# Optimization experiments

Measured on AMD Instinct MI355X. Metric: run time of the kernel, lower is better.

The kernel has to match this reference:

```python
import jax, jax.numpy as jnp
import numpy as np

B, T, D, SPAN = 4, 4096, 1024, 128


def _windowed_attention(q, k, v, span):
    # Causal sliding-window attention: position t attends to [max(0, t-span+1), t].
    # Tiled as blocks of size span: each query block attends to its own block
    # plus the previous block (exactly covers the window), avoiding any [T,T]
    # or per-timestep materialization.
    B, T, D = q.shape
    S = span
    nb = T // S  # T chosen divisible by span
    qb = q.reshape(B, nb, S, D)
    kb = k.reshape(B, nb, S, D)
    vb = v.reshape(B, nb, S, D)
    pad = jnp.zeros((B, 1, S, D), dtype=q.dtype)
    kk = jnp.concatenate([jnp.concatenate([pad, kb[:, :-1]], axis=1), kb], axis=2)  # [B,nb,2S,D]
    vv = jnp.concatenate([jnp.concatenate([pad, vb[:, :-1]], axis=1), vb], axis=2)  # [B,nb,2S,D]
    scale = 1.0 / jnp.sqrt(jnp.asarray(D, dtype=q.dtype))
    scores = jnp.einsum('bnqd,bnkd->bnqk', qb, kk) * scale  # [B,nb,S,2S]
    n_idx = jnp.arange(nb)[:, None, None]      # block index
    q_idx = jnp.arange(S)[None, :, None]       # query offset within block
    k_idx = jnp.arange(2 * S)[None, None, :]   # key offset in [prev|cur] pair
    rel = k_idx - S - q_idx                    # key_pos - query_pos
    # window: -span+1 <= rel <= 0; first block's "previous" half is padding -> mask it
    mask = (rel <= 0) & (rel > -S) & ((n_idx > 0) | (k_idx >= S))
    neg = jnp.asarray(jnp.finfo(scores.dtype).min, dtype=scores.dtype)
    scores = jnp.where(mask, scores, neg)
    w = jax.nn.softmax(scores, axis=-1)
    out = jnp.einsum('bnqk,bnkd->bnqd', w, vv)
    return out.reshape(B, T, D)


def setup_inputs() -> dict:
    key = jax.random.key(0)
    ks = jax.random.split(key, 7)
    s = 1.0 / np.sqrt(D)
    return {
        'x': jax.random.normal(ks[0], (B, T, D), dtype=jnp.float32),
        'Wq': jax.random.normal(ks[1], (D, D), dtype=jnp.float32) * s,
        'bq': jax.random.normal(ks[2], (D,), dtype=jnp.float32) * s,
        'Wk': jax.random.normal(ks[3], (D, D), dtype=jnp.float32) * s,
        'bk': jax.random.normal(ks[4], (D,), dtype=jnp.float32) * s,
        'Wv': jax.random.normal(ks[5], (D, D), dtype=jnp.float32) * s,
        'bv': jax.random.normal(ks[6], (D,), dtype=jnp.float32) * s,
        'span': SPAN,
    }


def reference(x, Wq, bq, Wk, bk, Wv, bv, span):
    # torch nn.Linear: y = x @ W.T + b
    q = jnp.einsum('btd,ed->bte', x, Wq) + bq
    k = jnp.einsum('btd,ed->bte', x, Wk) + bk
    v = jnp.einsum('btd,ed->bte', x, Wv) + bv
    return _windowed_attention(q, k, v, span)
```

## Files before the change

### kernel.cpp

```cpp
#include <hip/hip_runtime.h>
#include <hip/hip_bf16.h>

#define BB 4
#define TT 4096
#define DD 1024
#define SS 128
#define NBLK 32
#define MM (BB*TT)

typedef __attribute__((ext_vector_type(8))) short bf16x8;
typedef __attribute__((ext_vector_type(4))) short s16x4;
typedef __attribute__((ext_vector_type(4))) float f32x4;

#define VMCNT(N) asm volatile("s_waitcnt vmcnt(" #N ")" ::: "memory")

__device__ __forceinline__ void block_sync() {
    asm volatile("" ::: "memory");
    __builtin_amdgcn_s_barrier();
    asm volatile("" ::: "memory");
}

__device__ __forceinline__ short f2bf(float f) {
    union { float f; unsigned u; } cv; cv.f = f;
    unsigned u = cv.u;
    u += 0x7fffu + ((u >> 16) & 1u);
    return (short)(u >> 16);
}

__device__ __forceinline__ void gload16(const short* g, short* l) {
    __builtin_amdgcn_global_load_lds(
        (const __attribute__((address_space(1))) void*)g,
        (__attribute__((address_space(3))) void*)l, 16, 0, 0);
}

__global__ __launch_bounds__(256) void cast_f32_bf16(
    const float* __restrict__ src, short* __restrict__ dst)
{
    const int i = (blockIdx.x * 256 + threadIdx.x) * 4;
    const float4 v = *(const float4*)(src + i);
    s16x4 o;
    o.x = f2bf(v.x); o.y = f2bf(v.y); o.z = f2bf(v.z); o.w = f2bf(v.w);
    *(s16x4*)(dst + i) = o;
}

__global__ __launch_bounds__(256) void cast_w3(
    const float* __restrict__ a, const float* __restrict__ b,
    const float* __restrict__ c, short* __restrict__ dst)
{
    const float* src = (blockIdx.y == 0) ? a : (blockIdx.y == 1) ? b : c;
    short* d = dst + (size_t)blockIdx.y * DD * DD;
    const int i = (blockIdx.x * 256 + threadIdx.x) * 4;
    const float4 v = *(const float4*)(src + i);
    s16x4 o;
    o.x = f2bf(v.x); o.y = f2bf(v.y); o.z = f2bf(v.z); o.w = f2bf(v.w);
    *(s16x4*)(d + i) = o;
}

__global__ __launch_bounds__(256) void qkv_gemm(
    const short* __restrict__ X,
    const short* __restrict__ W3,
    const float* __restrict__ bq, const float* __restrict__ bk,
    const float* __restrict__ bv,
    short* __restrict__ q, short* __restrict__ k, short* __restrict__ vT)
{
    __shared__ short As[2][4096];
    __shared__ short Bs[2][4096];

    const int tid = threadIdx.x;
    const int l   = blockIdx.x;
    const int xcd = l & 7;
    const int rr  = l >> 3;
    const int m0  = (xcd * 16 + (rr & 15)) * 128;
    const int n_idx = rr >> 4;
    const int grp = n_idx >> 3;
    const int n0g = (n_idx & 7) * 128;

    const short* W = W3 + (size_t)grp * DD * DD;
    const float* bias = (grp == 0) ? bq : (grp == 1) ? bk : bv;

    const int wv   = tid >> 6, lane = tid & 63;
    const int wm   = wv >> 1,  wn   = wv & 1;
    const int quad = lane >> 4, c16 = lane & 15;
    const int srow = lane >> 2;
    const int scol = (lane & 3) * 8;

    auto stage = [&](int kk) {
        short* as = As[kk & 1];
        short* bs = Bs[kk & 1];
        const int k0 = kk * 32;
#pragma unroll
        for (int s = 0; s < 2; s++) {
            const int row = (wv * 2 + s) * 16 + srow;
            gload16(X + (m0 + row) * DD + k0 + scol, as + row * 32 + scol);
            gload16(W + (n0g + row) * DD + k0 + scol, bs + row * 32 + scol);
        }
    };

    f32x4 acc[4][4];
#pragma unroll
    for (int i = 0; i < 4; i++)
#pragma unroll
        for (int j = 0; j < 4; j++) acc[i][j] = (f32x4){0.f, 0.f, 0.f, 0.f};

    stage(0);

    if (grp != 2) {
        for (int kk = 0; kk < 32; kk++) {
            __syncthreads();
            if (kk < 31) stage(kk + 1);
            const short* as = As[kk & 1];
            const short* bs = Bs[kk & 1];
            bf16x8 af[4], bfr[4];
#pragma unroll
            for (int i = 0; i < 4; i++)
                af[i] = *(const bf16x8*)(as + (wm * 64 + i * 16 + c16) * 32 + quad * 8);
#pragma unroll
            for (int j = 0; j < 4; j++)
                bfr[j] = *(const bf16x8*)(bs + (wn * 64 + j * 16 + c16) * 32 + quad * 8);
#pragma unroll
            for (int i = 0; i < 4; i++)
#pragma unroll
                for (int j = 0; j < 4; j++)
                    acc[i][j] = __builtin_amdgcn_mfma_f32_16x16x32_bf16(af[i], bfr[j], acc[i][j], 0, 0, 0);
        }
        short* Y = (grp == 0) ? q : k;
#pragma unroll
        for (int j = 0; j < 4; j++) {
            const int col = n0g + wn * 64 + j * 16 + c16;
            const float bc = bias[col];
#pragma unroll
            for (int i = 0; i < 4; i++) {
                const int row = m0 + wm * 64 + i * 16 + quad * 4;
#pragma unroll
                for (int r = 0; r < 4; r++)
                    Y[(row + r) * DD + col] = f2bf(acc[i][j][r] + bc);
            }
        }
    } else {
        for (int kk = 0; kk < 32; kk++) {
            __syncthreads();
            if (kk < 31) stage(kk + 1);
            const short* as = As[kk & 1];
            const short* bs = Bs[kk & 1];
            bf16x8 af[4], bfr[4];
#pragma unroll
            for (int i = 0; i < 4; i++)
                af[i] = *(const bf16x8*)(as + (wm * 64 + i * 16 + c16) * 32 + quad * 8);
#pragma unroll
            for (int j = 0; j < 4; j++)
                bfr[j] = *(const bf16x8*)(bs + (wn * 64 + j * 16 + c16) * 32 + quad * 8);
#pragma unroll
            for (int i = 0; i < 4; i++)
#pragma unroll
                for (int j = 0; j < 4; j++)
                    acc[i][j] = __builtin_amdgcn_mfma_f32_16x16x32_bf16(bfr[j], af[i], acc[i][j], 0, 0, 0);
        }
        const int b  = m0 >> 12;
        const int t0 = m0 & 4095;
#pragma unroll
        for (int j = 0; j < 4; j++) {
#pragma unroll
            for (int r = 0; r < 4; r++) {
                const int drow = n0g + wn * 64 + j * 16 + quad * 4 + r;
                const float bc = bias[drow];
#pragma unroll
                for (int i = 0; i < 4; i++) {
                    const int tcol = t0 + wm * 64 + i * 16 + c16;
                    vT[(b * DD + drow) * TT + tcol] = f2bf(acc[i][j][r] + bc);
                }
            }
        }
    }
}

__global__ __launch_bounds__(256) void attn_fused(
    const short* __restrict__ Q,
    const short* __restrict__ Kb,
    const short* __restrict__ VT,
    float* __restrict__ O)
{
    __shared__ short lds[78336];

    const int l   = blockIdx.x;
    const int xcd = l & 7;
    const int rr  = l >> 3;
    const int n   = xcd * 4 + (rr & 3);
    const int qh  = (rr >> 2) & 1;
    const int b   = rr >> 3;

    const int tid  = threadIdx.x;
    const int wv   = tid >> 6, lane = tid & 63;
    const int quad = lane >> 4, c16 = lane & 15;
    const int srow = tid >> 2;
    const int scol = (tid & 3) * 8;

    const int qrow   = b * TT + n * SS + qh * 64;
    const int krow   = b * TT + n * SS - SS;
    const int bstart = b * TT;

    f32x4 acc[16];
#pragma unroll
    for (int j = 0; j < 16; j++) acc[j] = (f32x4){0.f, 0.f, 0.f, 0.f};

    auto stage1 = [&](int kk, int bi) {
        short* qb   = lds + bi * 20480;
        short* kbuf = qb + 4096;
        const int k0 = kk * 64;
#pragma unroll
        for (int ks = 0; ks < 2; ks++) {
            gload16(Q + (qrow + srow) * DD + k0 + ks * 32 + scol,
                    qb + ks * 2048 + srow * 32 + scol);
#pragma unroll
            for (int s = 0; s < 4; s++) {
                const int row = srow + s * 64;
                int g = krow + row;
                if (g < bstart) g = bstart;
                gload16(Kb + g * DD + k0 + ks * 32 + scol,
                        kbuf + ks * 8192 + row * 32 + scol);
            }
        }
    };

    stage1(0, 0);
    stage1(1, 1);
    for (int kk = 0; kk < 16; kk++) {
        if (kk < 15) { VMCNT(10); } else { VMCNT(0); }
        block_sync();
        if (kk < 14) stage1(kk + 2, (kk + 2) % 3);
        const short* qb   = lds + (kk % 3) * 20480;
        const short* kbuf = qb + 4096;
#pragma unroll
        for (int ks = 0; ks < 2; ks++) {
            bf16x8 a = *(const bf16x8*)(qb + ks * 2048 + (wv * 16 + c16) * 32 + quad * 8);
#pragma unroll
            for (int j = 0; j < 16; j++) {
                bf16x8 bf = *(const bf16x8*)(kbuf + ks * 8192 + (j * 16 + c16) * 32 + quad * 8);
                acc[j] = __builtin_amdgcn_mfma_f32_16x16x32_bf16(a, bf, acc[j], 0, 0, 0);
            }
        }
    }

    __syncthreads();

    const int tbase = n * SS - SS;
    auto stage2 = [&](int s, short* vbuf) {
        const int d0 = (s >> 1) * 128;
        const int kh = (s & 1) * 128;
#pragma unroll
        for (int kc = 0; kc < 4; kc++) {
#pragma unroll
            for (int s64 = 0; s64 < 2; s64++) {
                const int row = srow + s64 * 64;
                int t = tbase + kh + kc * 32 + scol;
                if (t < 0) t = 0;
                gload16(VT + (size_t)(b * DD + d0 + row) * TT + t,
                        vbuf + kc * 4096 + row * 32 + scol);
            }
        }
    };
    stage2(0, lds);
    stage2(1, lds + 16384);

    short* Pw = lds + 61440 + wv * (16 * 264);
    const float scale = 0.03125f;
#pragma unroll
    for (int r = 0; r < 4; r++) {
        const int q_idx = qh * 64 + wv * 16 + quad * 4 + r;
        float mx = -3.0e38f;
#pragma unroll
        for (int j = 0; j < 16; j++) {
            const int k_idx = j * 16 + c16;
            const int rel = k_idx - SS - q_idx;
            const bool valid = (rel <= 0) & (rel > -SS) & ((n > 0) | (k_idx >= SS));
            const float sv = valid ? acc[j][r] * scale : -3.0e38f;
            acc[j][r] = sv;
            mx = fmaxf(mx, sv);
        }
#pragma unroll
        for (int o = 1; o < 16; o <<= 1) mx = fmaxf(mx, __shfl_xor(mx, o));
        float sm = 0.f;
#pragma unroll
        for (int j = 0; j < 16; j++) {
            const float p = __expf(acc[j][r] - mx);
            acc[j][r] = p;
            sm += p;
        }
#pragma unroll
        for (int o = 1; o < 16; o <<= 1) sm += __shfl_xor(sm, o);
        const float inv = 1.0f / sm;
#pragma unroll
        for (int j = 0; j < 16; j++)
            Pw[(quad * 4 + r) * 264 + j * 16 + c16] = f2bf(acc[j][r] * inv);
    }

    f32x4 o8[8];
#pragma unroll
    for (int j = 0; j < 8; j++) o8[j] = (f32x4){0.f, 0.f, 0.f, 0.f};

    for (int s = 0; s < 16; s++) {
        if (s < 2)       { VMCNT(8); }
        else if (s < 15) { VMCNT(40); }
        else             { VMCNT(0); }
        block_sync();
        if (s < 14) stage2(s + 2, lds + ((s + 2) % 3) * 16384);
        const short* vbuf = lds + (s % 3) * 16384;
        const int kh = (s & 1) * 128;
#pragma unroll
        for (int kc = 0; kc < 4; kc++) {
            bf16x8 a = *(const bf16x8*)(Pw + c16 * 264 + kh + kc * 32 + quad * 8);
#pragma unroll
            for (int jj = 0; jj < 8; jj++) {
                bf16x8 bf = *(const bf16x8*)(vbuf + kc * 4096 + (jj * 16 + c16) * 32 + quad * 8);
                o8[jj] = __builtin_amdgcn_mfma_f32_16x16x32_bf16(a, bf, o8[jj], 0, 0, 0);
            }
        }
        if (s & 1) {
            const int d0 = (s >> 1) * 128;
#pragma unroll
            for (int jj = 0; jj < 8; jj++) {
#pragma unroll
                for (int r = 0; r < 4; r++)
                    O[(size_t)(qrow + wv * 16 + quad * 4 + r) * DD + d0 + jj * 16 + c16] = o8[jj][r];
                o8[jj] = (f32x4){0.f, 0.f, 0.f, 0.f};
            }
        }
    }
}

extern "C" void kernel_launch(void* const* d_in, const int* in_sizes, int n_in,
                              void* d_out, int out_size, void* d_ws, size_t ws_size,
                              hipStream_t stream) {
    const float* x  = (const float*)d_in[0];
    const float* Wq = (const float*)d_in[1];
    const float* bq = (const float*)d_in[2];
    const float* Wk = (const float*)d_in[3];
    const float* bk = (const float*)d_in[4];
    const float* Wv = (const float*)d_in[5];
    const float* bv = (const float*)d_in[6];
    float* out = (float*)d_out;

    char* ws = (char*)d_ws;
    const size_t SZ = (size_t)MM * DD * 2;
    short* q   = (short*)(ws);
    short* k   = (short*)(ws + SZ);
    short* vT  = (short*)(ws + 2 * SZ);
    short* xb  = (short*)(ws + 3 * SZ);
    short* w3b = (short*)(ws + 4 * SZ);

    dim3 blk(256);
    cast_f32_bf16<<<MM * DD / 1024, blk, 0, stream>>>(x, xb);
    cast_w3<<<dim3(DD * DD / 1024, 3), blk, 0, stream>>>(Wq, Wk, Wv, w3b);

    qkv_gemm<<<3072, blk, 0, stream>>>(xb, w3b, bq, bk, bv, q, k, vT);

    attn_fused<<<256, blk, 0, stream>>>(q, k, vT, out);
}
```

Before: 320.9 us.

## Rewrite QKV GEMM with 256x256 tiles, 8 waves, swizzled LDS and phased pipeline

Replaces the 128x128, 4-wave QKV projection GEMM with a templated 256x256-tile kernel using 512 threads, a 64-wide K step, XOR-swizzled LDS layout, and a four-phase schedule that interleaves async global-to-LDS staging with MFMA blocks under raised wave priority. Larger tiles raise arithmetic intensity and cut global traffic per FLOP, and the swizzle targets LDS bank conflicts. It also relaxes the final vmcnt wait in the attention kernel's last V stage from 0 to 16. The new GEMM uses many more accumulator registers and 128KB of LDS per block, and the relaxed wait could be unsafe if the outstanding loads are actually needed.

```diff
diff --git a/kernel.cpp b/kernel.cpp
--- a/kernel.cpp
+++ b/kernel.cpp
@@ -5,7 +5,6 @@
 #define TT 4096
 #define DD 1024
 #define SS 128
-#define NBLK 32
 #define MM (BB*TT)
 
 typedef __attribute__((ext_vector_type(8))) short bf16x8;
@@ -13,6 +12,7 @@
 typedef __attribute__((ext_vector_type(4))) float f32x4;
 
 #define VMCNT(N) asm volatile("s_waitcnt vmcnt(" #N ")" ::: "memory")
+#define LGKM0()  asm volatile("s_waitcnt lgkmcnt(0)" ::: "memory")
 
 __device__ __forceinline__ void block_sync() {
     asm volatile("" ::: "memory");
@@ -56,121 +56,168 @@
     *(s16x4*)(d + i) = o;
 }
 
-__global__ __launch_bounds__(256) void qkv_gemm(
-    const short* __restrict__ X,
-    const short* __restrict__ W3,
+
+#define MF(a_, b_, c_) ((GRP == 2)                                            \
+    ? __builtin_amdgcn_mfma_f32_16x16x32_bf16((b_), (a_), (c_), 0, 0, 0)      \
+    : __builtin_amdgcn_mfma_f32_16x16x32_bf16((a_), (b_), (c_), 0, 0, 0))
+
+#define QKV_PHASE(ABASE, P, STAGE_STMT, VM_STMT)                              \
+  do {                                                                        \
+    bf16x8 af0k0 = *(const bf16x8*)((ABASE) + (((P)*2)*16   + c16) * 64 + sw0);\
+    bf16x8 af0k1 = *(const bf16x8*)((ABASE) + (((P)*2)*16   + c16) * 64 + sw1);\
+    bf16x8 af1k0 = *(const bf16x8*)((ABASE) + (((P)*2+1)*16 + c16) * 64 + sw0);\
+    bf16x8 af1k1 = *(const bf16x8*)((ABASE) + (((P)*2+1)*16 + c16) * 64 + sw1);\
+    STAGE_STMT;                                                               \
+    block_sync();                                                             \
+    LGKM0();                                                                  \
+    __builtin_amdgcn_s_setprio(1);                                            \
+    _Pragma("unroll")                                                         \
+    for (int nj = 0; nj < 4; nj++) {                                          \
+      acc[(P)*2][nj]   = MF(af0k0, bf[nj][0], acc[(P)*2][nj]);                \
+      acc[(P)*2][nj]   = MF(af0k1, bf[nj][1], acc[(P)*2][nj]);                \
+      acc[(P)*2+1][nj] = MF(af1k0, bf[nj][0], acc[(P)*2+1][nj]);              \
+      acc[(P)*2+1][nj] = MF(af1k1, bf[nj][1], acc[(P)*2+1][nj]);              \
+    }                                                                         \
+    __builtin_amdgcn_s_setprio(0);                                            \
+    VM_STMT;                                                                  \
+    block_sync();                                                             \
+  } while (0)
+
+template<int GRP>
+__device__ __forceinline__ void qkv_core(
+    const short* __restrict__ X, const short* __restrict__ W,
+    const float* __restrict__ bias,
+    short* __restrict__ Y, short* __restrict__ vT,
+    short* lds, const int m_base, const int n_base)
+{
+    const int tid  = threadIdx.x;
+    const int wv   = tid >> 6, lane = tid & 63;
+    const int wm   = wv >> 2,  wn   = wv & 3;
+    const int quad = lane >> 4, c16 = lane & 15;
+    const int swz  = c16 & 7;
+    const int sw0  = ((quad)     ^ swz) * 8;
+    const int sw1  = ((quad + 4) ^ swz) * 8;
+
+    auto stageA = [&](int k0, int d, int h) {
+        short* dst = lds + d * 16384 + h * 8192;
+#pragma unroll
+        for (int g = 0; g < 2; g++) {
+            const int idx = g * 512 + tid;
+            const int row = idx >> 3, slot = idx & 7;
+            gload16(X + (size_t)(m_base + h * 128 + row) * DD + k0
+                      + ((slot ^ (row & 7)) * 8),
+                    dst + row * 64 + slot * 8);
+        }
+    };
+    auto stageB = [&](int k0, int d, int h) {
+        short* dst = lds + 32768 + d * 16384 + h * 8192;
+#pragma unroll
+        for (int g = 0; g < 2; g++) {
+            const int idx = g * 512 + tid;
+            const int row = idx >> 3, slot = idx & 7;
+            gload16(W + (size_t)(n_base + h * 128 + row) * DD + k0
+                      + ((slot ^ (row & 7)) * 8),
+                    dst + row * 64 + slot * 8);
+        }
+    };
+
+    f32x4 acc[8][4];
+#pragma unroll
+    for (int i = 0; i < 8; i++)
+#pragma unroll
+        for (int j = 0; j < 4; j++) acc[i][j] = (f32x4){0.f, 0.f, 0.f, 0.f};
+
+    stageA(0, 0, 0);  stageA(0, 0, 1);
+    stageB(0, 0, 0);  stageB(0, 0, 1);
+    stageB(64, 1, 0); stageB(64, 1, 1);
+    VMCNT(4);
+    block_sync();
+
+    const short* Abuf0 = lds + wm * 8192;
+    const short* Abuf1 = lds + 16384 + wm * 8192;
+    const short* Bbuf0 = lds + 32768 + (wn >> 1) * 8192 + (wn & 1) * 4096;
+    const short* Bbuf1 = lds + 49152 + (wn >> 1) * 8192 + (wn & 1) * 4096;
+
+    bf16x8 bf[4][2];
+
+    for (int it = 0; it < 8; ++it) {
+        const int k1 = it * 128 + 64;
+        const int k2 = it * 128 + 128;
+        const int k3 = it * 128 + 192;
+        const bool more = (it < 7);
+
+#pragma unroll
+        for (int nj = 0; nj < 4; nj++) {
+            bf[nj][0] = *(const bf16x8*)(Bbuf0 + (nj * 16 + c16) * 64 + sw0);
+            bf[nj][1] = *(const bf16x8*)(Bbuf0 + (nj * 16 + c16) * 64 + sw1);
+        }
+        QKV_PHASE(Abuf0, 0, stageA(k1, 1, 0), ((void)0));
+        QKV_PHASE(Abuf0, 1, stageA(k1, 1, 1), ((void)0));
+        QKV_PHASE(Abuf0, 2, if (more) stageB(k2, 0, 0), ((void)0));
+        QKV_PHASE(Abuf0, 3, if (more) stageB(k2, 0, 1),
+                  if (more) { VMCNT(4); } else { VMCNT(0); });
+
+#pragma unroll
+        for (int nj = 0; nj < 4; nj++) {
+            bf[nj][0] = *(const bf16x8*)(Bbuf1 + (nj * 16 + c16) * 64 + sw0);
+            bf[nj][1] = *(const bf16x8*)(Bbuf1 + (nj * 16 + c16) * 64 + sw1);
+        }
+        QKV_PHASE(Abuf1, 0, if (more) stageA(k2, 0, 0), ((void)0));
+        QKV_PHASE(Abuf1, 1, if (more) stageA(k2, 0, 1), ((void)0));
+        QKV_PHASE(Abuf1, 2, if (more) stageB(k3, 1, 0), ((void)0));
+        QKV_PHASE(Abuf1, 3, if (more) stageB(k3, 1, 1),
+                  if (more) { VMCNT(4); } else { VMCNT(0); });
+    }
+
+    if (GRP != 2) {
+#pragma unroll
+        for (int nj = 0; nj < 4; nj++) {
+            const int col = n_base + wn * 64 + nj * 16 + c16;
+            const float bc = bias[col];
+#pragma unroll
+            for (int mi = 0; mi < 8; mi++) {
+                const int row = m_base + wm * 128 + mi * 16 + quad * 4;
+#pragma unroll
+                for (int r = 0; r < 4; r++)
+                    Y[(size_t)(row + r) * DD + col] = f2bf(acc[mi][nj][r] + bc);
+            }
+        }
+    } else {
+#pragma unroll
+        for (int nj = 0; nj < 4; nj++) {
+#pragma unroll
+            for (int r = 0; r < 4; r++) {
+                const int drow = n_base + wn * 64 + nj * 16 + quad * 4 + r;
+                const float bc = bias[drow];
+#pragma unroll
+                for (int mi = 0; mi < 8; mi++) {
+                    const int mcol = m_base + wm * 128 + mi * 16 + c16;
+                    vT[((size_t)(mcol >> 12) * DD + drow) * TT + (mcol & 4095)]
+                        = f2bf(acc[mi][nj][r] + bc);
+                }
+            }
+        }
+    }
+}
+
+__global__ __launch_bounds__(512, 2) void qkv_gemm8(
+    const short* __restrict__ X, const short* __restrict__ W3,
     const float* __restrict__ bq, const float* __restrict__ bk,
     const float* __restrict__ bv,
     short* __restrict__ q, short* __restrict__ k, short* __restrict__ vT)
 {
-    __shared__ short As[2][4096];
-    __shared__ short Bs[2][4096];
-
-    const int tid = threadIdx.x;
-    const int l   = blockIdx.x;
-    const int xcd = l & 7;
-    const int rr  = l >> 3;
-    const int m0  = (xcd * 16 + (rr & 15)) * 128;
-    const int n_idx = rr >> 4;
-    const int grp = n_idx >> 3;
-    const int n0g = (n_idx & 7) * 128;
-
-    const short* W = W3 + (size_t)grp * DD * DD;
-    const float* bias = (grp == 0) ? bq : (grp == 1) ? bk : bv;
-
-    const int wv   = tid >> 6, lane = tid & 63;
-    const int wm   = wv >> 1,  wn   = wv & 1;
-    const int quad = lane >> 4, c16 = lane & 15;
-    const int srow = lane >> 2;
-    const int scol = (lane & 3) * 8;
-
-    auto stage = [&](int kk) {
-        short* as = As[kk & 1];
-        short* bs = Bs[kk & 1];
-        const int k0 = kk * 32;
-#pragma unroll
-        for (int s = 0; s < 2; s++) {
-            const int row = (wv * 2 + s) * 16 + srow;
-            gload16(X + (m0 + row) * DD + k0 + scol, as + row * 32 + scol);
-            gload16(W + (n0g + row) * DD + k0 + scol, bs + row * 32 + scol);
-        }
-    };
-
-    f32x4 acc[4][4];
-#pragma unroll
-    for (int i = 0; i < 4; i++)
-#pragma unroll
-        for (int j = 0; j < 4; j++) acc[i][j] = (f32x4){0.f, 0.f, 0.f, 0.f};
-
-    stage(0);
-
-    if (grp != 2) {
-        for (int kk = 0; kk < 32; kk++) {
-            __syncthreads();
-            if (kk < 31) stage(kk + 1);
-            const short* as = As[kk & 1];
-            const short* bs = Bs[kk & 1];
-            bf16x8 af[4], bfr[4];
-#pragma unroll
-            for (int i = 0; i < 4; i++)
-                af[i] = *(const bf16x8*)(as + (wm * 64 + i * 16 + c16) * 32 + quad * 8);
-#pragma unroll
-            for (int j = 0; j < 4; j++)
-                bfr[j] = *(const bf16x8*)(bs + (wn * 64 + j * 16 + c16) * 32 + quad * 8);
-#pragma unroll
-            for (int i = 0; i < 4; i++)
-#pragma unroll
-                for (int j = 0; j < 4; j++)
-                    acc[i][j] = __builtin_amdgcn_mfma_f32_16x16x32_bf16(af[i], bfr[j], acc[i][j], 0, 0, 0);
-        }
-        short* Y = (grp == 0) ? q : k;
-#pragma unroll
-        for (int j = 0; j < 4; j++) {
-            const int col = n0g + wn * 64 + j * 16 + c16;
-            const float bc = bias[col];
-#pragma unroll
-            for (int i = 0; i < 4; i++) {
-                const int row = m0 + wm * 64 + i * 16 + quad * 4;
-#pragma unroll
-                for (int r = 0; r < 4; r++)
-                    Y[(row + r) * DD + col] = f2bf(acc[i][j][r] + bc);
-            }
-        }
-    } else {
-        for (int kk = 0; kk < 32; kk++) {
-            __syncthreads();
-            if (kk < 31) stage(kk + 1);
-            const short* as = As[kk & 1];
-            const short* bs = Bs[kk & 1];
-            bf16x8 af[4], bfr[4];
-#pragma unroll
-            for (int i = 0; i < 4; i++)
-                af[i] = *(const bf16x8*)(as + (wm * 64 + i * 16 + c16) * 32 + quad * 8);
-#pragma unroll
-            for (int j = 0; j < 4; j++)
-                bfr[j] = *(const bf16x8*)(bs + (wn * 64 + j * 16 + c16) * 32 + quad * 8);
-#pragma unroll
-            for (int i = 0; i < 4; i++)
-#pragma unroll
-                for (int j = 0; j < 4; j++)
-                    acc[i][j] = __builtin_amdgcn_mfma_f32_16x16x32_bf16(bfr[j], af[i], acc[i][j], 0, 0, 0);
-        }
-        const int b  = m0 >> 12;
-        const int t0 = m0 & 4095;
-#pragma unroll
-        for (int j = 0; j < 4; j++) {
-#pragma unroll
-            for (int r = 0; r < 4; r++) {
-                const int drow = n0g + wn * 64 + j * 16 + quad * 4 + r;
-                const float bc = bias[drow];
-#pragma unroll
-                for (int i = 0; i < 4; i++) {
-                    const int tcol = t0 + wm * 64 + i * 16 + c16;
-                    vT[(b * DD + drow) * TT + tcol] = f2bf(acc[i][j][r] + bc);
-                }
-            }
-        }
-    }
+    __shared__ __align__(16) short lds[65536];
+    const int bid = blockIdx.x;
+    const int wg  = (bid & 7) * 96 + (bid >> 3);
+    const int mt  = wg & 63;
+    const int cn  = wg >> 6;
+    const int grp = cn >> 2;
+    const int nt  = cn & 3;
+    const int m_base = mt * 256;
+    const int n_base = nt * 256;
+    if (grp == 0)      qkv_core<0>(X, W3,              bq, q, nullptr, lds, m_base, n_base);
+    else if (grp == 1) qkv_core<1>(X, W3 + DD * DD,    bk, k, nullptr, lds, m_base, n_base);
+    else               qkv_core<2>(X, W3 + 2 * DD * DD, bv, nullptr, vT, lds, m_base, n_base);
 }
 
 __global__ __launch_bounds__(256) void attn_fused(
@@ -300,7 +347,7 @@
     for (int s = 0; s < 16; s++) {
         if (s < 2)       { VMCNT(8); }
         else if (s < 15) { VMCNT(40); }
-        else             { VMCNT(0); }
+        else             { VMCNT(16); }
         block_sync();
         if (s < 14) stage2(s + 2, lds + ((s + 2) % 3) * 16384);
         const short* vbuf = lds + (s % 3) * 16384;
@@ -351,7 +398,7 @@
     cast_f32_bf16<<<MM * DD / 1024, blk, 0, stream>>>(x, xb);
     cast_w3<<<dim3(DD * DD / 1024, 3), blk, 0, stream>>>(Wq, Wk, Wv, w3b);
 
-    qkv_gemm<<<3072, blk, 0, stream>>>(xb, w3b, bq, bk, bv, q, k, vT);
-
-    attn_fused<<<256, blk, 0, stream>>>(q, k, vT, out);
-}
+    qkv_gemm8<<<768, 512, 0, stream>>>(xb, w3b, bq, bk, bv, q, k, vT);
+
+    attn_fused<<<256, 256, 0, stream>>>(q, k, vT, out);
+}
```

New measurement: 300.2 us. 1.07x faster.
